# Kernel optimization log

Measured on AMD Instinct MI355X. Metric: run time of the kernel, lower is better.

The kernel has to match this reference:

```python
import jax, jax.numpy as jnp
import numpy as np

NUM_GRAPHS = 128
NODES_PER_GRAPH = 512
NUM_NODES = NUM_GRAPHS * NODES_PER_GRAPH
NUM_EDGES = NUM_NODES * 16
IN_DIM = 64
HID = 128
NUM_HEADS = 4
BN_EPS = 1e-5


def setup_inputs() -> dict:
    key = jax.random.key(0)
    ks = jax.random.split(key, 12)
    x = jax.random.normal(ks[0], (NUM_NODES, IN_DIM), dtype=jnp.float32)
    edge_index = jax.random.randint(ks[1], (2, NUM_EDGES), 0, NUM_NODES, dtype=jnp.int32)
    batch = jnp.repeat(jnp.arange(NUM_GRAPHS, dtype=jnp.int32), NODES_PER_GRAPH)
    s = 0.05
    W0 = jax.random.normal(ks[2], (IN_DIM, HID), dtype=jnp.float32) * s
    b0 = jnp.zeros((HID,), jnp.float32)
    Wh = jax.random.normal(ks[3], (3, HID, HID), dtype=jnp.float32) * s  # convs 1..3
    bh = jnp.zeros((3, HID), jnp.float32)
    bn_gamma = jnp.ones((4, HID), jnp.float32)
    bn_beta = jnp.zeros((4, HID), jnp.float32)
    bn_mean = jnp.zeros((4, HID), jnp.float32)
    bn_var = jnp.ones((4, HID), jnp.float32)
    attn_in_w = jax.random.normal(ks[4], (3 * HID, HID), dtype=jnp.float32) * s
    attn_in_b = jnp.zeros((3 * HID,), jnp.float32)
    attn_out_w = jax.random.normal(ks[5], (HID, HID), dtype=jnp.float32) * s
    attn_out_b = jnp.zeros((HID,), jnp.float32)
    return dict(x=x, W0=W0, b0=b0, Wh=Wh, bh=bh, bn_gamma=bn_gamma, bn_beta=bn_beta,
                bn_mean=bn_mean, bn_var=bn_var, attn_in_w=attn_in_w, attn_in_b=attn_in_b,
                attn_out_w=attn_out_w, attn_out_b=attn_out_b, edge_index=edge_index, batch=batch)


def _forward(x, W0, b0, Wh, bh, bn_gamma, bn_beta, bn_mean, bn_var,
             attn_in_w, attn_in_b, attn_out_w, attn_out_b, edge_index, batch):
    N = x.shape[0]
    src, dst = edge_index[0], edge_index[1]
    # GCN symmetric normalization with self-loops (PyG GCNConv)
    deg = jax.ops.segment_sum(jnp.ones_like(src, jnp.float32), dst, num_segments=N) + 1.0
    dis = jax.lax.rsqrt(deg)                      # deg^{-1/2}
    enorm = (dis[src] * dis[dst])[:, None]        # per-edge norm
    self_norm = (dis * dis)[:, None]              # self-loop norm

    def gcn(h, W, b):
        h = h @ W
        agg = jax.ops.segment_sum(h[src] * enorm, dst, num_segments=N)
        return agg + h * self_norm + b

    def bn(h, i):
        scale = bn_gamma[i] * jax.lax.rsqrt(bn_var[i] + BN_EPS)
        return (h - bn_mean[i]) * scale + bn_beta[i]  # eval-mode BN

    # dropout is identity in eval mode
    h = jax.nn.relu(bn(gcn(x, W0, b0), 0))
    h = jax.nn.relu(bn(gcn(h, Wh[0], bh[0]), 1))
    h = jax.nn.relu(bn(gcn(h, Wh[1], bh[1]), 2))
    f = jax.nn.relu(bn(gcn(h, Wh[2], bh[2]), 3))   # [N, HID]

    # per-graph self-attention (equal-size contiguous graphs -> batched MHA)
    dh = HID // NUM_HEADS
    xg = f.reshape(NUM_GRAPHS, NODES_PER_GRAPH, HID)
    qkv = xg @ attn_in_w.T + attn_in_b            # [G, n, 3H]
    q, k, v = jnp.split(qkv, 3, axis=-1)

    def heads(t):
        return t.reshape(NUM_GRAPHS, NODES_PER_GRAPH, NUM_HEADS, dh).transpose(0, 2, 1, 3)
    q, k, v = heads(q), heads(k), heads(v)
    scores = jnp.einsum('ghnd,ghmd->ghnm', q, k) / np.sqrt(dh).astype(np.float32)
    attn = jax.nn.softmax(scores, axis=-1)
    o = jnp.einsum('ghnm,ghmd->ghnd', attn, v).transpose(0, 2, 1, 3).reshape(NUM_GRAPHS, NODES_PER_GRAPH, HID)
    o = o @ attn_out_w.T + attn_out_b
    final = o.reshape(N, HID)

    # global mean pool over batch indices
    cnt = jax.ops.segment_sum(jnp.ones((N,), jnp.float32), batch, num_segments=NUM_GRAPHS)
    graph_emb = jax.ops.segment_sum(final, batch, num_segments=NUM_GRAPHS) / cnt[:, None]
    return final, graph_emb


def reference(x, W0, b0, Wh, bh, bn_gamma, bn_beta, bn_mean, bn_var,
              attn_in_w, attn_in_b, attn_out_w, attn_out_b, edge_index, batch):
    return _forward(x, W0, b0, Wh, bh, bn_gamma, bn_beta, bn_mean, bn_var,
                    attn_in_w, attn_in_b, attn_out_w, attn_out_b, edge_index, batch)
```

## Files before the change

kernel.cpp:

```cpp
#include <hip/hip_runtime.h>
#include <hip/hip_bf16.h>
#include <cstdint>
#include <cstddef>

#define N_NODES 65536
#define N_EDGES 1048576
#define N_GRAPHS 128
#define NPG 512
#define IN_DIM 64
#define HID 128
#define BN_EPS 1e-5f

typedef __attribute__((ext_vector_type(8))) short bf16x8;
typedef __attribute__((ext_vector_type(4))) float f32x4;
typedef __attribute__((ext_vector_type(8))) unsigned short u16x8;
typedef __attribute__((ext_vector_type(4))) unsigned short u16x4;

__device__ inline unsigned short f2bf(float f) {
  unsigned u = __builtin_bit_cast(unsigned, f);
  u = u + 0x7fffu + ((u >> 16) & 1u);
  return (unsigned short)(u >> 16);
}
__device__ inline float bf2f(unsigned short h) {
  unsigned u = ((unsigned)h) << 16;
  return __builtin_bit_cast(float, u);
}
__device__ inline void split_bf(float v, unsigned short& hi, unsigned short& lo) {
  hi = f2bf(v);
  lo = f2bf(v - bf2f(hi));
}
__device__ inline bf16x8 ld_bf8(const unsigned short* p) {
  u16x4 a = *(const u16x4*)p;
  u16x4 b = *(const u16x4*)(p + 4);
  u16x8 r = __builtin_shufflevector(a, b, 0, 1, 2, 3, 4, 5, 6, 7);
  return __builtin_bit_cast(bf16x8, r);
}

__global__ __launch_bounds__(256) void hist_kernel(const int* __restrict__ dst,
                                                   int* __restrict__ deg) {
  int e = blockIdx.x * 256 + threadIdx.x;
  if (e < N_EDGES) atomicAdd(&deg[dst[e]], 1);
}

__global__ __launch_bounds__(256) void dis_kernel(const int* __restrict__ deg,
                                                  float* __restrict__ dis) {
  int n = blockIdx.x * 256 + threadIdx.x;
  if (n < N_NODES) dis[n] = 1.0f / sqrtf((float)deg[n] + 1.0f);
}

__global__ __launch_bounds__(1024) void scan_kernel(const int* __restrict__ deg,
                                                    int* __restrict__ offsets,
                                                    int* __restrict__ cursor) {
  __shared__ int sums[1024];
  int t = threadIdx.x;
  int base = t * 64;
  const int4* dp = (const int4*)(deg + base);
  int s = 0;
#pragma unroll
  for (int i = 0; i < 16; i++) {
    int4 v = dp[i];
    s += v.x + v.y + v.z + v.w;
  }
  sums[t] = s;
  __syncthreads();
  for (int off = 1; off < 1024; off <<= 1) {
    int v = (t >= off) ? sums[t - off] : 0;
    __syncthreads();
    sums[t] += v;
    __syncthreads();
  }
  int run = (t == 0) ? 0 : sums[t - 1];
#pragma unroll
  for (int i = 0; i < 16; i++) {
    int4 v = dp[i];
    int idx = base + i * 4;
    offsets[idx] = run; cursor[idx] = run; run += v.x;
    offsets[idx + 1] = run; cursor[idx + 1] = run; run += v.y;
    offsets[idx + 2] = run; cursor[idx + 2] = run; run += v.z;
    offsets[idx + 3] = run; cursor[idx + 3] = run; run += v.w;
  }
  if (t == 1023) offsets[N_NODES] = run;
}

__global__ __launch_bounds__(256) void fill_kernel(const int* __restrict__ src,
                                                   const int* __restrict__ dst,
                                                   const float* __restrict__ dis,
                                                   int* __restrict__ cursor,
                                                   int* __restrict__ csr,
                                                   float* __restrict__ wedge) {
  int e = blockIdx.x * 256 + threadIdx.x;
  if (e < N_EDGES) {
    int d = dst[e];
    int s = src[e];
    int slot = atomicAdd(&cursor[d], 1);
    csr[slot] = s;
    wedge[slot] = dis[s] * dis[d];
  }
}

__global__ __launch_bounds__(256) void agg64_kernel(const float* __restrict__ x,
                                                    const float* __restrict__ dis,
                                                    const float* __restrict__ wedge,
                                                    const int* __restrict__ offsets,
                                                    const int* __restrict__ csr,
                                                    unsigned short* __restrict__ zhi,
                                                    unsigned short* __restrict__ zlo) {
  int node = blockIdx.x * 4 + (threadIdx.x >> 6);
  int lane = threadIdx.x & 63;
  float dn = dis[node];
  float acc = x[(size_t)node * 64 + lane] * dn * dn;
  int beg = offsets[node], end = offsets[node + 1];
  int k = beg;
  for (; k + 8 <= end; k += 8) {
    int s[8];
    float w[8], v[8];
#pragma unroll
    for (int i = 0; i < 8; i++) {
      s[i] = csr[k + i];
      w[i] = wedge[k + i];
    }
#pragma unroll
    for (int i = 0; i < 8; i++) v[i] = x[(size_t)s[i] * 64 + lane];
#pragma unroll
    for (int i = 0; i < 8; i++) acc = fmaf(w[i], v[i], acc);
  }
  for (; k + 4 <= end; k += 4) {
    int s0 = csr[k], s1 = csr[k + 1], s2 = csr[k + 2], s3 = csr[k + 3];
    float w0 = wedge[k], w1 = wedge[k + 1], w2 = wedge[k + 2], w3 = wedge[k + 3];
    float v0 = x[(size_t)s0 * 64 + lane];
    float v1 = x[(size_t)s1 * 64 + lane];
    float v2 = x[(size_t)s2 * 64 + lane];
    float v3 = x[(size_t)s3 * 64 + lane];
    acc = fmaf(w0, v0, acc);
    acc = fmaf(w1, v1, acc);
    acc = fmaf(w2, v2, acc);
    acc = fmaf(w3, v3, acc);
  }
  for (; k < end; k++) {
    int s = csr[k];
    acc = fmaf(wedge[k], x[(size_t)s * 64 + lane], acc);
  }
  unsigned short h_, l_;
  split_bf(acc, h_, l_);
  zhi[(size_t)node * 64 + lane] = h_;
  zlo[(size_t)node * 64 + lane] = l_;
}

__global__ __launch_bounds__(256) void agg128_kernel(const float* __restrict__ h,
                                                     const float* __restrict__ dis,
                                                     const float* __restrict__ wedge,
                                                     const int* __restrict__ offsets,
                                                     const int* __restrict__ csr,
                                                     unsigned short* __restrict__ zhi,
                                                     unsigned short* __restrict__ zlo) {
  int node = blockIdx.x * 4 + (threadIdx.x >> 6);
  int lane = threadIdx.x & 63;
  float dn = dis[node];
  float sn = dn * dn;
  const float* hr = h + (size_t)node * 128;
  float a0 = hr[lane] * sn;
  float a1 = hr[lane + 64] * sn;
  int beg = offsets[node], end = offsets[node + 1];
  int k = beg;
  for (; k + 8 <= end; k += 8) {
    int s[8];
    float w[8], u[8], d[8];
#pragma unroll
    for (int i = 0; i < 8; i++) {
      s[i] = csr[k + i];
      w[i] = wedge[k + i];
    }
#pragma unroll
    for (int i = 0; i < 8; i++) {
      const float* p = h + (size_t)s[i] * 128;
      u[i] = p[lane];
      d[i] = p[lane + 64];
    }
#pragma unroll
    for (int i = 0; i < 8; i++) {
      a0 = fmaf(w[i], u[i], a0);
      a1 = fmaf(w[i], d[i], a1);
    }
  }
  for (; k + 4 <= end; k += 4) {
    int s0 = csr[k], s1 = csr[k + 1], s2 = csr[k + 2], s3 = csr[k + 3];
    float w0 = wedge[k], w1 = wedge[k + 1], w2 = wedge[k + 2], w3 = wedge[k + 3];
    const float* p0 = h + (size_t)s0 * 128;
    const float* p1 = h + (size_t)s1 * 128;
    const float* p2 = h + (size_t)s2 * 128;
    const float* p3 = h + (size_t)s3 * 128;
    float u0 = p0[lane], d0 = p0[lane + 64];
    float u1 = p1[lane], d1 = p1[lane + 64];
    float u2 = p2[lane], d2 = p2[lane + 64];
    float u3 = p3[lane], d3 = p3[lane + 64];
    a0 = fmaf(w0, u0, a0); a1 = fmaf(w0, d0, a1);
    a0 = fmaf(w1, u1, a0); a1 = fmaf(w1, d1, a1);
    a0 = fmaf(w2, u2, a0); a1 = fmaf(w2, d2, a1);
    a0 = fmaf(w3, u3, a0); a1 = fmaf(w3, d3, a1);
  }
  for (; k < end; k++) {
    int s = csr[k];
    float wt = wedge[k];
    const float* hs = h + (size_t)s * 128;
    a0 = fmaf(wt, hs[lane], a0);
    a1 = fmaf(wt, hs[lane + 64], a1);
  }
  unsigned short h0, l0, h1, l1;
  split_bf(a0, h0, l0);
  split_bf(a1, h1, l1);
  zhi[(size_t)node * 128 + lane] = h0;
  zlo[(size_t)node * 128 + lane] = l0;
  zhi[(size_t)node * 128 + lane + 64] = h1;
  zlo[(size_t)node * 128 + lane + 64] = l1;
}

template <bool TRANS>
__global__ __launch_bounds__(256) void wprep_kernel(const float* __restrict__ W, int K, int O,
                                                    unsigned short* __restrict__ hi,
                                                    unsigned short* __restrict__ lo) {
  int idx = blockIdx.x * 256 + threadIdx.x;
  int KC = K / 32;
  int total = (O / 16) * KC * 64;
  if (idx >= total) return;
  int lane = idx & 63;
  int rest = idx >> 6;
  int kc = rest % KC;
  int nt = rest / KC;
  int n = nt * 16 + (lane & 15);
  int kb = kc * 32 + (lane >> 4) * 8;
  unsigned short* hp = hi + (size_t)idx * 8;
  unsigned short* lp = lo + (size_t)idx * 8;
#pragma unroll
  for (int j = 0; j < 8; j++) {
    int k = kb + j;
    float v = TRANS ? W[(size_t)n * K + k] : W[(size_t)k * O + n];
    unsigned short h_, l_;
    split_bf(v, h_, l_);
    hp[j] = h_;
    lp[j] = l_;
  }
}

template <int K, int O, bool DOBN, bool DORELU, bool SPLIT_OUT>
__global__ __launch_bounds__(256) void gemm_mfma(
    const unsigned short* __restrict__ Ahi, const unsigned short* __restrict__ Alo,
    const unsigned short* __restrict__ Whi, const unsigned short* __restrict__ Wlo,
    const float* __restrict__ bias,
    const float* __restrict__ gamma, const float* __restrict__ beta,
    const float* __restrict__ mean, const float* __restrict__ var,
    float* __restrict__ Cf, unsigned short* __restrict__ Chi,
    unsigned short* __restrict__ Clo) {
  constexpr int KC = K / 32;
  int wave = threadIdx.x >> 6;
  int lane = threadIdx.x & 63;
  int m0 = blockIdx.x * 128 + wave * 32;
  int o0 = blockIdx.y * 128;
  int mrow = lane & 15;
  int kseg = (lane >> 4) * 8;

  f32x4 acc[2][8];
#pragma unroll
  for (int mt = 0; mt < 2; mt++)
#pragma unroll
    for (int nt = 0; nt < 8; nt++) acc[mt][nt] = (f32x4)0.0f;

#pragma unroll
  for (int kc = 0; kc < KC; kc++) {
    bf16x8 ah[2], al[2];
#pragma unroll
    for (int mt = 0; mt < 2; mt++) {
      size_t aoff = (size_t)(m0 + mt * 16 + mrow) * K + kc * 32 + kseg;
      ah[mt] = *(const bf16x8*)(Ahi + aoff);
      al[mt] = *(const bf16x8*)(Alo + aoff);
    }
#pragma unroll
    for (int nt = 0; nt < 8; nt++) {
      size_t foff = (((size_t)(blockIdx.y * 8 + nt) * KC + kc) * 64 + lane) * 8;
      bf16x8 bh = *(const bf16x8*)(Whi + foff);
      bf16x8 bl = *(const bf16x8*)(Wlo + foff);
#pragma unroll
      for (int mt = 0; mt < 2; mt++) {
        acc[mt][nt] = __builtin_amdgcn_mfma_f32_16x16x32_bf16(ah[mt], bh, acc[mt][nt], 0, 0, 0);
        acc[mt][nt] = __builtin_amdgcn_mfma_f32_16x16x32_bf16(ah[mt], bl, acc[mt][nt], 0, 0, 0);
        acc[mt][nt] = __builtin_amdgcn_mfma_f32_16x16x32_bf16(al[mt], bh, acc[mt][nt], 0, 0, 0);
      }
    }
  }

  int ccol = lane & 15;
  int crow0 = (lane >> 4) * 4;
#pragma unroll
  for (int nt = 0; nt < 8; nt++) {
    int c = o0 + nt * 16 + ccol;
    float sc, cb;
    float b = bias[c];
    if (DOBN) {
      sc = gamma[c] * rsqrtf(var[c] + BN_EPS);
      cb = (b - mean[c]) * sc + beta[c];
    } else {
      sc = 1.0f;
      cb = b;
    }
#pragma unroll
    for (int mt = 0; mt < 2; mt++) {
#pragma unroll
      for (int r = 0; r < 4; r++) {
        float v = fmaf(acc[mt][nt][r], sc, cb);
        if (DORELU) v = fmaxf(v, 0.0f);
        size_t row = (size_t)(m0 + mt * 16 + crow0 + r);
        if (SPLIT_OUT) {
          unsigned short h_, l_;
          split_bf(v, h_, l_);
          Chi[row * O + c] = h_;
          Clo[row * O + c] = l_;
        } else {
          Cf[row * O + c] = v;
        }
      }
    }
  }
}

__global__ __launch_bounds__(256) void knorm_kernel(const float* __restrict__ qkv,
                                                    float* __restrict__ kmax2) {
  int g = blockIdx.x >> 2;
  int h = blockIdx.x & 3;
  size_t gbase = (size_t)g * NPG;
  float best = 0.0f;
#pragma unroll
  for (int r = 0; r < 2; r++) {
    int j = r * 256 + threadIdx.x;
    const float* kp = &qkv[(gbase + j) * 384 + 128 + h * 32];
    float s = 0.0f;
#pragma unroll
    for (int i = 0; i < 8; i++) {
      float4 v = *(const float4*)(kp + i * 4);
      s = fmaf(v.x, v.x, s);
      s = fmaf(v.y, v.y, s);
      s = fmaf(v.z, v.z, s);
      s = fmaf(v.w, v.w, s);
    }
    best = fmaxf(best, s);
  }
#pragma unroll
  for (int off = 32; off >= 1; off >>= 1)
    best = fmaxf(best, __shfl_xor(best, off, 64));
  __shared__ float red[4];
  int wave = threadIdx.x >> 6;
  if ((threadIdx.x & 63) == 0) red[wave] = best;
  __syncthreads();
  if (threadIdx.x == 0) {
    float m = fmaxf(fmaxf(red[0], red[1]), fmaxf(red[2], red[3]));
    kmax2[blockIdx.x] = m;
  }
}

__global__ __launch_bounds__(256, 2) void attn_mfma_kernel(
    const float* __restrict__ qkv, const float* __restrict__ kmax2,
    unsigned short* __restrict__ ohi, unsigned short* __restrict__ olo) {
  int b = blockIdx.x;
  int g = b >> 3;
  int h = (b >> 1) & 3;
  int half = b & 1;
  int t = threadIdx.x;
  int wave = t >> 6;
  int lane = t & 63;
  int quad = lane >> 4;
  int l15 = lane & 15;
  size_t gbase = (size_t)g * NPG;
  int qb = half * 256 + wave * 64;

  const float cf = 0.17677669529663687f * 1.4426950408889634f;

  __shared__ unsigned short Kh[32][36], Kl[32][36];
  __shared__ unsigned short Vh[33][36], Vl[33][36];
  __shared__ char wbuf[4][9472] __attribute__((aligned(16)));

  unsigned short* Ph = (unsigned short*)wbuf[wave];
  unsigned short* Pl = Ph + 64 * 36;
  float* Ot = (float*)wbuf[wave];

  bf16x8 qh[4], ql[4];
  float qn2p[4];
#pragma unroll
  for (int mt = 0; mt < 4; mt++) {
    const float* qp = &qkv[(gbase + qb + mt * 16 + l15) * 384 + h * 32 + quad * 8];
    float4 f0 = *(const float4*)qp;
    float4 f1 = *(const float4*)(qp + 4);
    float v[8] = {f0.x * cf, f0.y * cf, f0.z * cf, f0.w * cf,
                  f1.x * cf, f1.y * cf, f1.z * cf, f1.w * cf};
    u16x8 hh, ll;
    float s = 0.0f;
#pragma unroll
    for (int j = 0; j < 8; j++) {
      unsigned short hi_, lo_;
      split_bf(v[j], hi_, lo_);
      hh[j] = hi_;
      ll[j] = lo_;
      s = fmaf(v[j], v[j], s);
    }
    qh[mt] = __builtin_bit_cast(bf16x8, hh);
    ql[mt] = __builtin_bit_cast(bf16x8, ll);
    s += __shfl_xor(s, 16);
    s += __shfl_xor(s, 32);
    qn2p[mt] = s;
  }
  if (quad == 0) {
#pragma unroll
    for (int mt = 0; mt < 4; mt++) Ot[mt * 16 + l15] = qn2p[mt];
  }
  float km2 = kmax2[g * 4 + h];
  float Mq[4][4];
#pragma unroll
  for (int mt = 0; mt < 4; mt++)
#pragma unroll
    for (int r = 0; r < 4; r++)
      Mq[mt][r] = sqrtf(Ot[mt * 16 + quad * 4 + r] * km2);

  f32x4 Oa[4][3];
#pragma unroll
  for (int mt = 0; mt < 4; mt++)
#pragma unroll
    for (int nt = 0; nt < 3; nt++) Oa[mt][nt] = (f32x4)0.0f;

  for (int c = 0; c < 16; c++) {
    __syncthreads();
    if (t >= 128) {
      int t2 = t - 128;
      int key = t2 >> 2;
      int ds = (t2 & 3) * 8;
      const float* kp = &qkv[(gbase + (size_t)(c * 32 + key)) * 384 + 128 + h * 32 + ds];
      float4 f0 = *(const float4*)kp;
      float4 f1 = *(const float4*)(kp + 4);
      float v[8] = {f0.x, f0.y, f0.z, f0.w, f1.x, f1.y, f1.z, f1.w};
      u16x4 h0, h1, l0, l1;
#pragma unroll
      for (int j = 0; j < 4; j++) {
        unsigned short hi_, lo_;
        split_bf(v[j], hi_, lo_);
        h0[j] = hi_; l0[j] = lo_;
        split_bf(v[j + 4], hi_, lo_);
        h1[j] = hi_; l1[j] = lo_;
      }
      *(u16x4*)&Kh[key][ds] = h0;
      *(u16x4*)&Kh[key][ds + 4] = h1;
      *(u16x4*)&Kl[key][ds] = l0;
      *(u16x4*)&Kl[key][ds + 4] = l1;
    } else if (t < 64) {
      int keyb = (t & 7) * 4;
      int dvb = (t >> 3) * 4;
      float4 r0 = *(const float4*)&qkv[(gbase + (size_t)(c * 32 + keyb + 0)) * 384 + 256 + h * 32 + dvb];
      float4 r1 = *(const float4*)&qkv[(gbase + (size_t)(c * 32 + keyb + 1)) * 384 + 256 + h * 32 + dvb];
      float4 r2 = *(const float4*)&qkv[(gbase + (size_t)(c * 32 + keyb + 2)) * 384 + 256 + h * 32 + dvb];
      float4 r3 = *(const float4*)&qkv[(gbase + (size_t)(c * 32 + keyb + 3)) * 384 + 256 + h * 32 + dvb];
      float rr[4][4] = {{r0.x, r0.y, r0.z, r0.w}, {r1.x, r1.y, r1.z, r1.w},
                        {r2.x, r2.y, r2.z, r2.w}, {r3.x, r3.y, r3.z, r3.w}};
#pragma unroll
      for (int c2 = 0; c2 < 4; c2++) {
        ushort4 hv, lv;
        unsigned short hi_, lo_;
        split_bf(rr[0][c2], hi_, lo_); hv.x = hi_; lv.x = lo_;
        split_bf(rr[1][c2], hi_, lo_); hv.y = hi_; lv.y = lo_;
        split_bf(rr[2][c2], hi_, lo_); hv.z = hi_; lv.z = lo_;
        split_bf(rr[3][c2], hi_, lo_); hv.w = hi_; lv.w = lo_;
        *(ushort4*)&Vh[dvb + c2][keyb] = hv;
        *(ushort4*)&Vl[dvb + c2][keyb] = lv;
      }
    } else if (t < 68) {
      int i = t - 64;
      u16x8 ones;
#pragma unroll
      for (int j = 0; j < 8; j++) ones[j] = 0x3F80;
      *(u16x4*)&Vh[32][i * 8] = __builtin_shufflevector(ones, ones, 0, 1, 2, 3);
      *(u16x4*)&Vh[32][i * 8 + 4] = __builtin_shufflevector(ones, ones, 4, 5, 6, 7);
    }
    __syncthreads();

#pragma unroll
    for (int nt = 0; nt < 2; nt++) {
      bf16x8 bkh = ld_bf8(&Kh[nt * 16 + l15][quad * 8]);
      bf16x8 bkl = ld_bf8(&Kl[nt * 16 + l15][quad * 8]);
#pragma unroll
      for (int mt = 0; mt < 4; mt++) {
        f32x4 S = (f32x4)0.0f;
        S = __builtin_amdgcn_mfma_f32_16x16x32_bf16(qh[mt], bkh, S, 0, 0, 0);
        S = __builtin_amdgcn_mfma_f32_16x16x32_bf16(qh[mt], bkl, S, 0, 0, 0);
        S = __builtin_amdgcn_mfma_f32_16x16x32_bf16(ql[mt], bkh, S, 0, 0, 0);
#pragma unroll
        for (int r = 0; r < 4; r++) {
          float p = __builtin_exp2f(S[r] - Mq[mt][r]);
          unsigned short hi_, lo_;
          split_bf(p, hi_, lo_);
          int row = mt * 16 + quad * 4 + r;
          Ph[row * 36 + nt * 16 + l15] = hi_;
          Pl[row * 36 + nt * 16 + l15] = lo_;
        }
      }
    }
    bf16x8 pah[4], pal[4];
#pragma unroll
    for (int mt = 0; mt < 4; mt++) {
      pah[mt] = ld_bf8(&Ph[(mt * 16 + l15) * 36 + quad * 8]);
      pal[mt] = ld_bf8(&Pl[(mt * 16 + l15) * 36 + quad * 8]);
    }
#pragma unroll
    for (int nt = 0; nt < 3; nt++) {
      bf16x8 bvh = ld_bf8(&Vh[nt * 16 + l15][quad * 8]);
      if (nt < 2) {
        bf16x8 bvl = ld_bf8(&Vl[nt * 16 + l15][quad * 8]);
#pragma unroll
        for (int mt = 0; mt < 4; mt++) {
          Oa[mt][nt] = __builtin_amdgcn_mfma_f32_16x16x32_bf16(pah[mt], bvh, Oa[mt][nt], 0, 0, 0);
          Oa[mt][nt] = __builtin_amdgcn_mfma_f32_16x16x32_bf16(pah[mt], bvl, Oa[mt][nt], 0, 0, 0);
          Oa[mt][nt] = __builtin_amdgcn_mfma_f32_16x16x32_bf16(pal[mt], bvh, Oa[mt][nt], 0, 0, 0);
        }
      } else {
#pragma unroll
        for (int mt = 0; mt < 4; mt++) {
          Oa[mt][nt] = __builtin_amdgcn_mfma_f32_16x16x32_bf16(pah[mt], bvh, Oa[mt][nt], 0, 0, 0);
          Oa[mt][nt] = __builtin_amdgcn_mfma_f32_16x16x32_bf16(pal[mt], bvh, Oa[mt][nt], 0, 0, 0);
        }
      }
    }
  }

#pragma unroll
  for (int mt = 0; mt < 4; mt++) {
#pragma unroll
    for (int r = 0; r < 4; r++) {
      int row = mt * 16 + quad * 4 + r;
      Ot[row * 37 + l15] = Oa[mt][0][r];
      Ot[row * 37 + 16 + l15] = Oa[mt][1][r];
      if (l15 == 0) Ot[row * 37 + 32] = Oa[mt][2][r];
    }
  }
  {
    int row = lane;
    float inv = 1.0f / Ot[row * 37 + 32];
    size_t node = gbase + qb + row;
    u16x8 vh, vl;
#pragma unroll
    for (int seg = 0; seg < 4; seg++) {
#pragma unroll
      for (int j = 0; j < 8; j++) {
        unsigned short hi_, lo_;
        split_bf(Ot[row * 37 + seg * 8 + j] * inv, hi_, lo_);
        vh[j] = hi_;
        vl[j] = lo_;
      }
      *(u16x8*)(ohi + node * 128 + h * 32 + seg * 8) = vh;
      *(u16x8*)(olo + node * 128 + h * 32 + seg * 8) = vl;
    }
  }
}

__global__ __launch_bounds__(128) void pool_kernel(const float* __restrict__ fin,
                                                   float* __restrict__ emb) {
  int g = blockIdx.x, c = threadIdx.x;
  const float* p = fin + (size_t)g * NPG * HID + c;
  float s = 0.0f;
  for (int i = 0; i < NPG; i++) s += p[(size_t)i * HID];
  emb[g * HID + c] = s * (1.0f / NPG);
}

extern "C" void kernel_launch(void* const* d_in, const int* in_sizes, int n_in,
                              void* d_out, int out_size, void* d_ws, size_t ws_size,
                              hipStream_t stream) {
  (void)in_sizes; (void)n_in; (void)out_size; (void)ws_size;
  const float* x          = (const float*)d_in[0];
  const float* W0         = (const float*)d_in[1];
  const float* b0         = (const float*)d_in[2];
  const float* Wh         = (const float*)d_in[3];
  const float* bh         = (const float*)d_in[4];
  const float* bn_gamma   = (const float*)d_in[5];
  const float* bn_beta    = (const float*)d_in[6];
  const float* bn_mean    = (const float*)d_in[7];
  const float* bn_var     = (const float*)d_in[8];
  const float* attn_in_w  = (const float*)d_in[9];
  const float* attn_in_b  = (const float*)d_in[10];
  const float* attn_out_w = (const float*)d_in[11];
  const float* attn_out_b = (const float*)d_in[12];
  const int* edge_index   = (const int*)d_in[13];
  const int* src = edge_index;
  const int* dst = edge_index + N_EDGES;

  char* ws = (char*)d_ws;
  size_t off = 0;
  auto alloc = [&](size_t bytes) -> void* {
    void* p = ws + off;
    off += (bytes + 255) & ~(size_t)255;
    return p;
  };
  int*   deg     = (int*)alloc((size_t)N_NODES * 4);
  int*   offsets = (int*)alloc((size_t)(N_NODES + 1) * 4);
  int*   cursor  = (int*)alloc((size_t)N_NODES * 4);
  int*   csr     = (int*)alloc((size_t)N_EDGES * 4);
  float* wedge   = (float*)alloc((size_t)N_EDGES * 4);
  float* dis     = (float*)alloc((size_t)N_NODES * 4);
  float* bufA    = (float*)alloc((size_t)N_NODES * HID * 4);
  unsigned short* zhi = (unsigned short*)alloc((size_t)N_NODES * HID * 2);
  unsigned short* zlo = (unsigned short*)alloc((size_t)N_NODES * HID * 2);
  float* qkvb    = (float*)alloc((size_t)N_NODES * 384 * 4);
  float* kmax2   = (float*)alloc((size_t)N_GRAPHS * 4 * 4);
  unsigned short* w0h = (unsigned short*)alloc(8192 * 2);
  unsigned short* w0l = (unsigned short*)alloc(8192 * 2);
  unsigned short* whh[3], *whl[3];
  for (int i = 0; i < 3; i++) {
    whh[i] = (unsigned short*)alloc(16384 * 2);
    whl[i] = (unsigned short*)alloc(16384 * 2);
  }
  unsigned short* wqh = (unsigned short*)alloc(49152 * 2);
  unsigned short* wql = (unsigned short*)alloc(49152 * 2);
  unsigned short* woh = (unsigned short*)alloc(16384 * 2);
  unsigned short* wol = (unsigned short*)alloc(16384 * 2);

  unsigned short* fhi = (unsigned short*)bufA;
  unsigned short* flo = fhi + (size_t)N_NODES * HID;

  float* fin = (float*)d_out;
  float* emb = fin + (size_t)N_NODES * HID;

  hipMemsetAsync(deg, 0, (size_t)N_NODES * 4, stream);
  hist_kernel<<<N_EDGES / 256, 256, 0, stream>>>(dst, deg);
  dis_kernel<<<N_NODES / 256, 256, 0, stream>>>(deg, dis);
  scan_kernel<<<1, 1024, 0, stream>>>(deg, offsets, cursor);
  fill_kernel<<<N_EDGES / 256, 256, 0, stream>>>(src, dst, dis, cursor, csr, wedge);

  wprep_kernel<false><<<4, 256, 0, stream>>>(W0, 64, 128, w0h, w0l);
  for (int i = 0; i < 3; i++)
    wprep_kernel<false><<<8, 256, 0, stream>>>(Wh + (size_t)i * HID * HID, 128, 128,
                                               whh[i], whl[i]);
  wprep_kernel<true><<<24, 256, 0, stream>>>(attn_in_w, 128, 384, wqh, wql);
  wprep_kernel<true><<<8, 256, 0, stream>>>(attn_out_w, 128, 128, woh, wol);

  dim3 ggrid(N_NODES / 128, 1);
  agg64_kernel<<<N_NODES / 4, 256, 0, stream>>>(x, dis, wedge, offsets, csr, zhi, zlo);
  gemm_mfma<64, 128, true, true, false><<<ggrid, 256, 0, stream>>>(
      zhi, zlo, w0h, w0l, b0, bn_gamma, bn_beta, bn_mean, bn_var, bufA, nullptr, nullptr);
  for (int L = 0; L < 2; L++) {
    agg128_kernel<<<N_NODES / 4, 256, 0, stream>>>(bufA, dis, wedge, offsets, csr, zhi, zlo);
    gemm_mfma<128, 128, true, true, false><<<ggrid, 256, 0, stream>>>(
        zhi, zlo, whh[L], whl[L], bh + (size_t)L * HID,
        bn_gamma + (size_t)(L + 1) * HID, bn_beta + (size_t)(L + 1) * HID,
        bn_mean + (size_t)(L + 1) * HID, bn_var + (size_t)(L + 1) * HID,
        bufA, nullptr, nullptr);
  }
  agg128_kernel<<<N_NODES / 4, 256, 0, stream>>>(bufA, dis, wedge, offsets, csr, zhi, zlo);
  gemm_mfma<128, 128, true, true, true><<<ggrid, 256, 0, stream>>>(
      zhi, zlo, whh[2], whl[2], bh + (size_t)2 * HID,
      bn_gamma + (size_t)3 * HID, bn_beta + (size_t)3 * HID,
      bn_mean + (size_t)3 * HID, bn_var + (size_t)3 * HID,
      nullptr, fhi, flo);
  dim3 qgrid(N_NODES / 128, 3);
  gemm_mfma<128, 384, false, false, false><<<qgrid, 256, 0, stream>>>(
      fhi, flo, wqh, wql, attn_in_b, nullptr, nullptr, nullptr, nullptr,
      qkvb, nullptr, nullptr);
  knorm_kernel<<<N_GRAPHS * 4, 256, 0, stream>>>(qkvb, kmax2);
  attn_mfma_kernel<<<N_GRAPHS * 4 * 2, 256, 0, stream>>>(qkvb, kmax2, zhi, zlo);
  gemm_mfma<128, 128, false, false, false><<<ggrid, 256, 0, stream>>>(
      zhi, zlo, woh, wol, attn_out_b, nullptr, nullptr, nullptr, nullptr,
      fin, nullptr, nullptr);
  pool_kernel<<<N_GRAPHS, 128, 0, stream>>>(fin, emb);
}
```

Baseline: 841.9 us.

## Emit QKV as pre-split fp16 hi/lo pairs and switch attention MFMAs to fp16

The QKV projection GEMM now writes each output as an fp16 hi/lo pair instead of fp32. The knorm and attention kernels load these pairs directly, so they no longer split fp32 into bf16 pairs on every K/V tile load. The attention MFMAs and the probability split now use fp16, and the softmax scale is folded into an fma with the max bound. This removes repeated conversion work and keeps QKV traffic the same size, but fp16's narrower exponent range risks overflow or underflow that bf16 would have handled.

Result: no change. 843.8 us (+0.2%).

```diff
diff --git a/kernel.cpp b/kernel.cpp
--- a/kernel.cpp
+++ b/kernel.cpp
@@ -12,6 +12,7 @@
 #define BN_EPS 1e-5f
 
 typedef __attribute__((ext_vector_type(8))) short bf16x8;
+typedef __attribute__((ext_vector_type(8))) _Float16 f16x8;
 typedef __attribute__((ext_vector_type(4))) float f32x4;
 typedef __attribute__((ext_vector_type(8))) unsigned short u16x8;
 typedef __attribute__((ext_vector_type(4))) unsigned short u16x4;
@@ -28,12 +29,24 @@
 __device__ inline void split_bf(float v, unsigned short& hi, unsigned short& lo) {
   hi = f2bf(v);
   lo = f2bf(v - bf2f(hi));
+}
+__device__ inline void split_f16(float v, unsigned short& hi, unsigned short& lo) {
+  _Float16 h = (_Float16)v;
+  _Float16 l = (_Float16)(v - (float)h);
+  hi = __builtin_bit_cast(unsigned short, h);
+  lo = __builtin_bit_cast(unsigned short, l);
 }
 __device__ inline bf16x8 ld_bf8(const unsigned short* p) {
   u16x4 a = *(const u16x4*)p;
   u16x4 b = *(const u16x4*)(p + 4);
   u16x8 r = __builtin_shufflevector(a, b, 0, 1, 2, 3, 4, 5, 6, 7);
   return __builtin_bit_cast(bf16x8, r);
+}
+__device__ inline f16x8 ld_f16x8(const unsigned short* p) {
+  u16x4 a = *(const u16x4*)p;
+  u16x4 b = *(const u16x4*)(p + 4);
+  u16x8 r = __builtin_shufflevector(a, b, 0, 1, 2, 3, 4, 5, 6, 7);
+  return __builtin_bit_cast(f16x8, r);
 }
 
 __global__ __launch_bounds__(256) void hist_kernel(const int* __restrict__ dst,
@@ -241,7 +254,7 @@
   }
 }
 
-template <int K, int O, bool DOBN, bool DORELU, bool SPLIT_OUT>
+template <int K, int O, bool DOBN, bool DORELU, int OUTMODE>
 __global__ __launch_bounds__(256) void gemm_mfma(
     const unsigned short* __restrict__ Ahi, const unsigned short* __restrict__ Alo,
     const unsigned short* __restrict__ Whi, const unsigned short* __restrict__ Wlo,
@@ -308,9 +321,14 @@
         float v = fmaf(acc[mt][nt][r], sc, cb);
         if (DORELU) v = fmaxf(v, 0.0f);
         size_t row = (size_t)(m0 + mt * 16 + crow0 + r);
-        if (SPLIT_OUT) {
+        if (OUTMODE == 1) {
           unsigned short h_, l_;
           split_bf(v, h_, l_);
+          Chi[row * O + c] = h_;
+          Clo[row * O + c] = l_;
+        } else if (OUTMODE == 3) {
+          unsigned short h_, l_;
+          split_f16(v, h_, l_);
           Chi[row * O + c] = h_;
           Clo[row * O + c] = l_;
         } else {
@@ -321,7 +339,8 @@
   }
 }
 
-__global__ __launch_bounds__(256) void knorm_kernel(const float* __restrict__ qkv,
+__global__ __launch_bounds__(256) void knorm_kernel(const unsigned short* __restrict__ qsh,
+                                                    const unsigned short* __restrict__ qsl,
                                                     float* __restrict__ kmax2) {
   int g = blockIdx.x >> 2;
   int h = blockIdx.x & 3;
@@ -330,15 +349,17 @@
 #pragma unroll
   for (int r = 0; r < 2; r++) {
     int j = r * 256 + threadIdx.x;
-    const float* kp = &qkv[(gbase + j) * 384 + 128 + h * 32];
+    size_t base = (gbase + j) * 384 + 128 + h * 32;
     float s = 0.0f;
 #pragma unroll
-    for (int i = 0; i < 8; i++) {
-      float4 v = *(const float4*)(kp + i * 4);
-      s = fmaf(v.x, v.x, s);
-      s = fmaf(v.y, v.y, s);
-      s = fmaf(v.z, v.z, s);
-      s = fmaf(v.w, v.w, s);
+    for (int i = 0; i < 4; i++) {
+      f16x8 hv = ld_f16x8(qsh + base + i * 8);
+      f16x8 lv = ld_f16x8(qsl + base + i * 8);
+#pragma unroll
+      for (int q = 0; q < 8; q++) {
+        float kvf = (float)hv[q] + (float)lv[q];
+        s = fmaf(kvf, kvf, s);
+      }
     }
     best = fmaxf(best, s);
   }
@@ -356,7 +377,8 @@
 }
 
 __global__ __launch_bounds__(256, 2) void attn_mfma_kernel(
-    const float* __restrict__ qkv, const float* __restrict__ kmax2,
+    const unsigned short* __restrict__ qsh, const unsigned short* __restrict__ qsl,
+    const float* __restrict__ kmax2,
     unsigned short* __restrict__ ohi, unsigned short* __restrict__ olo) {
   int b = blockIdx.x;
   int g = b >> 3;
@@ -370,7 +392,7 @@
   size_t gbase = (size_t)g * NPG;
   int qb = half * 256 + wave * 64;
 
-  const float cf = 0.17677669529663687f * 1.4426950408889634f;
+  const float cfl = 0.17677669529663687f * 1.4426950408889634f;
 
   __shared__ unsigned short Kh[32][36], Kl[32][36];
   __shared__ unsigned short Vh[33][36], Vl[33][36];
@@ -380,27 +402,21 @@
   unsigned short* Pl = Ph + 64 * 36;
   float* Ot = (float*)wbuf[wave];
 
-  bf16x8 qh[4], ql[4];
+  f16x8 qh[4], ql[4];
   float qn2p[4];
 #pragma unroll
   for (int mt = 0; mt < 4; mt++) {
-    const float* qp = &qkv[(gbase + qb + mt * 16 + l15) * 384 + h * 32 + quad * 8];
-    float4 f0 = *(const float4*)qp;
-    float4 f1 = *(const float4*)(qp + 4);
-    float v[8] = {f0.x * cf, f0.y * cf, f0.z * cf, f0.w * cf,
-                  f1.x * cf, f1.y * cf, f1.z * cf, f1.w * cf};
-    u16x8 hh, ll;
+    size_t base = (gbase + qb + mt * 16 + l15) * 384 + h * 32 + quad * 8;
+    u16x8 hu = *(const u16x8*)(qsh + base);
+    u16x8 lu = *(const u16x8*)(qsl + base);
+    qh[mt] = __builtin_bit_cast(f16x8, hu);
+    ql[mt] = __builtin_bit_cast(f16x8, lu);
     float s = 0.0f;
 #pragma unroll
     for (int j = 0; j < 8; j++) {
-      unsigned short hi_, lo_;
-      split_bf(v[j], hi_, lo_);
-      hh[j] = hi_;
-      ll[j] = lo_;
-      s = fmaf(v[j], v[j], s);
-    }
-    qh[mt] = __builtin_bit_cast(bf16x8, hh);
-    ql[mt] = __builtin_bit_cast(bf16x8, ll);
+      float q = (float)qh[mt][j] + (float)ql[mt][j];
+      s = fmaf(q, q, s);
+    }
     s += __shfl_xor(s, 16);
     s += __shfl_xor(s, 32);
     qn2p[mt] = s;
@@ -415,7 +431,7 @@
   for (int mt = 0; mt < 4; mt++)
 #pragma unroll
     for (int r = 0; r < 4; r++)
-      Mq[mt][r] = sqrtf(Ot[mt * 16 + quad * 4 + r] * km2);
+      Mq[mt][r] = cfl * sqrtf(Ot[mt * 16 + quad * 4 + r] * km2);
 
   f32x4 Oa[4][3];
 #pragma unroll
@@ -429,96 +445,85 @@
       int t2 = t - 128;
       int key = t2 >> 2;
       int ds = (t2 & 3) * 8;
-      const float* kp = &qkv[(gbase + (size_t)(c * 32 + key)) * 384 + 128 + h * 32 + ds];
-      float4 f0 = *(const float4*)kp;
-      float4 f1 = *(const float4*)(kp + 4);
-      float v[8] = {f0.x, f0.y, f0.z, f0.w, f1.x, f1.y, f1.z, f1.w};
-      u16x4 h0, h1, l0, l1;
-#pragma unroll
-      for (int j = 0; j < 4; j++) {
-        unsigned short hi_, lo_;
-        split_bf(v[j], hi_, lo_);
-        h0[j] = hi_; l0[j] = lo_;
-        split_bf(v[j + 4], hi_, lo_);
-        h1[j] = hi_; l1[j] = lo_;
-      }
-      *(u16x4*)&Kh[key][ds] = h0;
-      *(u16x4*)&Kh[key][ds + 4] = h1;
-      *(u16x4*)&Kl[key][ds] = l0;
-      *(u16x4*)&Kl[key][ds + 4] = l1;
+      size_t base = (gbase + (size_t)(c * 32 + key)) * 384 + 128 + h * 32 + ds;
+      u16x8 hu = *(const u16x8*)(qsh + base);
+      u16x8 lu = *(const u16x8*)(qsl + base);
+      *(u16x4*)&Kh[key][ds] = __builtin_shufflevector(hu, hu, 0, 1, 2, 3);
+      *(u16x4*)&Kh[key][ds + 4] = __builtin_shufflevector(hu, hu, 4, 5, 6, 7);
+      *(u16x4*)&Kl[key][ds] = __builtin_shufflevector(lu, lu, 0, 1, 2, 3);
+      *(u16x4*)&Kl[key][ds + 4] = __builtin_shufflevector(lu, lu, 4, 5, 6, 7);
     } else if (t < 64) {
       int keyb = (t & 7) * 4;
       int dvb = (t >> 3) * 4;
-      float4 r0 = *(const float4*)&qkv[(gbase + (size_t)(c * 32 + keyb + 0)) * 384 + 256 + h * 32 + dvb];
-      float4 r1 = *(const float4*)&qkv[(gbase + (size_t)(c * 32 + keyb + 1)) * 384 + 256 + h * 32 + dvb];
-      float4 r2 = *(const float4*)&qkv[(gbase + (size_t)(c * 32 + keyb + 2)) * 384 + 256 + h * 32 + dvb];
-      float4 r3 = *(const float4*)&qkv[(gbase + (size_t)(c * 32 + keyb + 3)) * 384 + 256 + h * 32 + dvb];
-      float rr[4][4] = {{r0.x, r0.y, r0.z, r0.w}, {r1.x, r1.y, r1.z, r1.w},
-                        {r2.x, r2.y, r2.z, r2.w}, {r3.x, r3.y, r3.z, r3.w}};
+      u16x4 h0, h1, h2, h3, l0, l1, l2, l3;
+      {
+        size_t r0 = (gbase + (size_t)(c * 32 + keyb + 0)) * 384 + 256 + h * 32 + dvb;
+        size_t r1 = (gbase + (size_t)(c * 32 + keyb + 1)) * 384 + 256 + h * 32 + dvb;
+        size_t r2 = (gbase + (size_t)(c * 32 + keyb + 2)) * 384 + 256 + h * 32 + dvb;
+        size_t r3 = (gbase + (size_t)(c * 32 + keyb + 3)) * 384 + 256 + h * 32 + dvb;
+        h0 = *(const u16x4*)(qsh + r0); l0 = *(const u16x4*)(qsl + r0);
+        h1 = *(const u16x4*)(qsh + r1); l1 = *(const u16x4*)(qsl + r1);
+        h2 = *(const u16x4*)(qsh + r2); l2 = *(const u16x4*)(qsl + r2);
+        h3 = *(const u16x4*)(qsh + r3); l3 = *(const u16x4*)(qsl + r3);
+      }
 #pragma unroll
       for (int c2 = 0; c2 < 4; c2++) {
-        ushort4 hv, lv;
-        unsigned short hi_, lo_;
-        split_bf(rr[0][c2], hi_, lo_); hv.x = hi_; lv.x = lo_;
-        split_bf(rr[1][c2], hi_, lo_); hv.y = hi_; lv.y = lo_;
-        split_bf(rr[2][c2], hi_, lo_); hv.z = hi_; lv.z = lo_;
-        split_bf(rr[3][c2], hi_, lo_); hv.w = hi_; lv.w = lo_;
-        *(ushort4*)&Vh[dvb + c2][keyb] = hv;
-        *(ushort4*)&Vl[dvb + c2][keyb] = lv;
+        u16x4 hv = {h0[c2], h1[c2], h2[c2], h3[c2]};
+        u16x4 lv = {l0[c2], l1[c2], l2[c2], l3[c2]};
+        *(u16x4*)&Vh[dvb + c2][keyb] = hv;
+        *(u16x4*)&Vl[dvb + c2][keyb] = lv;
       }
     } else if (t < 68) {
       int i = t - 64;
-      u16x8 ones;
-#pragma unroll
-      for (int j = 0; j < 8; j++) ones[j] = 0x3F80;
-      *(u16x4*)&Vh[32][i * 8] = __builtin_shufflevector(ones, ones, 0, 1, 2, 3);
-      *(u16x4*)&Vh[32][i * 8 + 4] = __builtin_shufflevector(ones, ones, 4, 5, 6, 7);
+      u16x4 ones = {0x3C00, 0x3C00, 0x3C00, 0x3C00};
+      *(u16x4*)&Vh[32][i * 8] = ones;
+      *(u16x4*)&Vh[32][i * 8 + 4] = ones;
     }
     __syncthreads();
 
 #pragma unroll
     for (int nt = 0; nt < 2; nt++) {
-      bf16x8 bkh = ld_bf8(&Kh[nt * 16 + l15][quad * 8]);
-      bf16x8 bkl = ld_bf8(&Kl[nt * 16 + l15][quad * 8]);
+      f16x8 bkh = ld_f16x8(&Kh[nt * 16 + l15][quad * 8]);
+      f16x8 bkl = ld_f16x8(&Kl[nt * 16 + l15][quad * 8]);
 #pragma unroll
       for (int mt = 0; mt < 4; mt++) {
         f32x4 S = (f32x4)0.0f;
-        S = __builtin_amdgcn_mfma_f32_16x16x32_bf16(qh[mt], bkh, S, 0, 0, 0);
-        S = __builtin_amdgcn_mfma_f32_16x16x32_bf16(qh[mt], bkl, S, 0, 0, 0);
-        S = __builtin_amdgcn_mfma_f32_16x16x32_bf16(ql[mt], bkh, S, 0, 0, 0);
+        S = __builtin_amdgcn_mfma_f32_16x16x32_f16(qh[mt], bkh, S, 0, 0, 0);
+        S = __builtin_amdgcn_mfma_f32_16x16x32_f16(qh[mt], bkl, S, 0, 0, 0);
+        S = __builtin_amdgcn_mfma_f32_16x16x32_f16(ql[mt], bkh, S, 0, 0, 0);
 #pragma unroll
         for (int r = 0; r < 4; r++) {
-          float p = __builtin_exp2f(S[r] - Mq[mt][r]);
+          float p = __builtin_exp2f(fmaf(S[r], cfl, -Mq[mt][r]));
           unsigned short hi_, lo_;
-          split_bf(p, hi_, lo_);
+          split_f16(p, hi_, lo_);
           int row = mt * 16 + quad * 4 + r;
           Ph[row * 36 + nt * 16 + l15] = hi_;
           Pl[row * 36 + nt * 16 + l15] = lo_;
         }
       }
     }
-    bf16x8 pah[4], pal[4];
+    f16x8 pah[4], pal[4];
 #pragma unroll
     for (int mt = 0; mt < 4; mt++) {
-      pah[mt] = ld_bf8(&Ph[(mt * 16 + l15) * 36 + quad * 8]);
-      pal[mt] = ld_bf8(&Pl[(mt * 16 + l15) * 36 + quad * 8]);
+      pah[mt] = ld_f16x8(&Ph[(mt * 16 + l15) * 36 + quad * 8]);
+      pal[mt] = ld_f16x8(&Pl[(mt * 16 + l15) * 36 + quad * 8]);
     }
 #pragma unroll
     for (int nt = 0; nt < 3; nt++) {
-      bf16x8 bvh = ld_bf8(&Vh[nt * 16 + l15][quad * 8]);
+      f16x8 bvh = ld_f16x8(&Vh[nt * 16 + l15][quad * 8]);
       if (nt < 2) {
-        bf16x8 bvl = ld_bf8(&Vl[nt * 16 + l15][quad * 8]);
+        f16x8 bvl = ld_f16x8(&Vl[nt * 16 + l15][quad * 8]);
 #pragma unroll
         for (int mt = 0; mt < 4; mt++) {
-          Oa[mt][nt] = __builtin_amdgcn_mfma_f32_16x16x32_bf16(pah[mt], bvh, Oa[mt][nt], 0, 0, 0);
-          Oa[mt][nt] = __builtin_amdgcn_mfma_f32_16x16x32_bf16(pah[mt], bvl, Oa[mt][nt], 0, 0, 0);
-          Oa[mt][nt] = __builtin_amdgcn_mfma_f32_16x16x32_bf16(pal[mt], bvh, Oa[mt][nt], 0, 0, 0);
+          Oa[mt][nt] = __builtin_amdgcn_mfma_f32_16x16x32_f16(pah[mt], bvh, Oa[mt][nt], 0, 0, 0);
+          Oa[mt][nt] = __builtin_amdgcn_mfma_f32_16x16x32_f16(pah[mt], bvl, Oa[mt][nt], 0, 0, 0);
+          Oa[mt][nt] = __builtin_amdgcn_mfma_f32_16x16x32_f16(pal[mt], bvh, Oa[mt][nt], 0, 0, 0);
         }
       } else {
 #pragma unroll
         for (int mt = 0; mt < 4; mt++) {
-          Oa[mt][nt] = __builtin_amdgcn_mfma_f32_16x16x32_bf16(pah[mt], bvh, Oa[mt][nt], 0, 0, 0);
-          Oa[mt][nt] = __builtin_amdgcn_mfma_f32_16x16x32_bf16(pal[mt], bvh, Oa[mt][nt], 0, 0, 0);
+          Oa[mt][nt] = __builtin_amdgcn_mfma_f32_16x16x32_f16(pah[mt], bvh, Oa[mt][nt], 0, 0, 0);
+          Oa[mt][nt] = __builtin_amdgcn_mfma_f32_16x16x32_f16(pal[mt], bvh, Oa[mt][nt], 0, 0, 0);
         }
       }
     }
@@ -600,7 +605,8 @@
   float* bufA    = (float*)alloc((size_t)N_NODES * HID * 4);
   unsigned short* zhi = (unsigned short*)alloc((size_t)N_NODES * HID * 2);
   unsigned short* zlo = (unsigned short*)alloc((size_t)N_NODES * HID * 2);
-  float* qkvb    = (float*)alloc((size_t)N_NODES * 384 * 4);
+  unsigned short* qsh = (unsigned short*)alloc((size_t)N_NODES * 384 * 2);
+  unsigned short* qsl = (unsigned short*)alloc((size_t)N_NODES * 384 * 2);
   float* kmax2   = (float*)alloc((size_t)N_GRAPHS * 4 * 4);
   unsigned short* w0h = (unsigned short*)alloc(8192 * 2);
   unsigned short* w0l = (unsigned short*)alloc(8192 * 2);
@@ -635,29 +641,29 @@
 
   dim3 ggrid(N_NODES / 128, 1);
   agg64_kernel<<<N_NODES / 4, 256, 0, stream>>>(x, dis, wedge, offsets, csr, zhi, zlo);
-  gemm_mfma<64, 128, true, true, false><<<ggrid, 256, 0, stream>>>(
+  gemm_mfma<64, 128, true, true, 0><<<ggrid, 256, 0, stream>>>(
       zhi, zlo, w0h, w0l, b0, bn_gamma, bn_beta, bn_mean, bn_var, bufA, nullptr, nullptr);
   for (int L = 0; L < 2; L++) {
     agg128_kernel<<<N_NODES / 4, 256, 0, stream>>>(bufA, dis, wedge, offsets, csr, zhi, zlo);
-    gemm_mfma<128, 128, true, true, false><<<ggrid, 256, 0, stream>>>(
+    gemm_mfma<128, 128, true, true, 0><<<ggrid, 256, 0, stream>>>(
         zhi, zlo, whh[L], whl[L], bh + (size_t)L * HID,
         bn_gamma + (size_t)(L + 1) * HID, bn_beta + (size_t)(L + 1) * HID,
         bn_mean + (size_t)(L + 1) * HID, bn_var + (size_t)(L + 1) * HID,
         bufA, nullptr, nullptr);
   }
   agg128_kernel<<<N_NODES / 4, 256, 0, stream>>>(bufA, dis, wedge, offsets, csr, zhi, zlo);
-  gemm_mfma<128, 128, true, true, true><<<ggrid, 256, 0, stream>>>(
+  gemm_mfma<128, 128, true, true, 1><<<ggrid, 256, 0, stream>>>(
       zhi, zlo, whh[2], whl[2], bh + (size_t)2 * HID,
       bn_gamma + (size_t)3 * HID, bn_beta + (size_t)3 * HID,
       bn_mean + (size_t)3 * HID, bn_var + (size_t)3 * HID,
       nullptr, fhi, flo);
   dim3 qgrid(N_NODES / 128, 3);
-  gemm_mfma<128, 384, false, false, false><<<qgrid, 256, 0, stream>>>(
+  gemm_mfma<128, 384, false, false, 3><<<qgrid, 256, 0, stream>>>(
       fhi, flo, wqh, wql, attn_in_b, nullptr, nullptr, nullptr, nullptr,
-      qkvb, nullptr, nullptr);
-  knorm_kernel<<<N_GRAPHS * 4, 256, 0, stream>>>(qkvb, kmax2);
-  attn_mfma_kernel<<<N_GRAPHS * 4 * 2, 256, 0, stream>>>(qkvb, kmax2, zhi, zlo);
-  gemm_mfma<128, 128, false, false, false><<<ggrid, 256, 0, stream>>>(
+      nullptr, qsh, qsl);
+  knorm_kernel<<<N_GRAPHS * 4, 256, 0, stream>>>(qsh, qsl, kmax2);
+  attn_mfma_kernel<<<N_GRAPHS * 4 * 2, 256, 0, stream>>>(qsh, qsl, kmax2, zhi, zlo);
+  gemm_mfma<128, 128, false, false, 0><<<ggrid, 256, 0, stream>>>(
       zhi, zlo, woh, wol, attn_out_b, nullptr, nullptr, nullptr, nullptr,
       fin, nullptr, nullptr);
   pool_kernel<<<N_GRAPHS, 128, 0, stream>>>(fin, emb);
```
